# Performance work log

Measured on AMD Instinct MI355X. Metric: run time of the kernel, lower is better.

The kernel has to match this reference:

```python
import jax, jax.numpy as jnp
import numpy as np

D_IN = 256
DIMS = 256


def setup_inputs() -> dict:
    key = jax.random.key(0)
    k1, k2, k3, k4, k5 = jax.random.split(key, 5)
    B, Tq, Tk = 4, 512, 512
    query = jax.random.normal(k1, (B, Tq, D_IN), dtype=jnp.float32)
    value = jax.random.normal(k2, (B, Tk, D_IN), dtype=jnp.float32)
    # Dense(dims, use_bias=False) kernels (glorot-like scale) and AdditiveAttention scale vector
    Wq = jax.random.normal(k3, (D_IN, DIMS), dtype=jnp.float32) / np.sqrt(D_IN)
    Wv = jax.random.normal(k4, (D_IN, DIMS), dtype=jnp.float32) / np.sqrt(D_IN)
    scale = jax.random.normal(k5, (DIMS,), dtype=jnp.float32)
    return {"query": query, "value": value, "Wq": Wq, "Wv": Wv, "scale": scale}


def reference(query, value, Wq, Wv, scale):
    # q_proj: [B,Tq,d], k_proj: [B,Tk,d]; attention value = RAW value tensor (as in source)
    q = jnp.einsum("bqi,id->bqd", query, Wq)
    k = jnp.einsum("bki,id->bkd", value, Wv)
    # Additive (Bahdanau) scores: [B,Tq,Tk] via broadcast tanh then reduce with scale
    scores = jnp.einsum("bqkd,d->bqk", jnp.tanh(q[:, :, None, :] + k[:, None, :, :]), scale)
    attn = jax.nn.softmax(scores, axis=-1)  # masks are all-ones -> no-op
    out = jnp.einsum("bqk,bki->bqi", attn, value)
    return out, attn
```

## Files before the change

### kernel.cpp

```cpp
#include <hip/hip_runtime.h>

#define LOG2E 1.4426950408889634f
#define TWO_LOG2E 2.885390081777927f

__device__ __forceinline__ float fast_exp2(float x) { return __builtin_amdgcn_exp2f(x); }
__device__ __forceinline__ float fast_rcp(float x)  { return __builtin_amdgcn_rcpf(x); }

__global__ __launch_bounds__(256) void proj_kernel(
    const float* __restrict__ query, const float* __restrict__ value,
    const float* __restrict__ Wq, const float* __restrict__ Wv,
    float* __restrict__ eq, float* __restrict__ ek)
{
    __shared__ float in_lds[8 * 256];
    const int t = threadIdx.x;
    const int row0 = blockIdx.x * 8;
    const float* src; const float* W; float* dst;
    if (row0 < 2048) { src = query + (size_t)row0 * 256; W = Wq; dst = eq + (size_t)row0 * 256; }
    else { const int r = row0 - 2048; src = value + (size_t)r * 256; W = Wv; dst = ek + (size_t)r * 256; }

    const float4* s4 = (const float4*)src;
    float4* l4 = (float4*)in_lds;
    l4[t] = s4[t];
    l4[t + 256] = s4[t + 256];
    __syncthreads();

    float acc[8];
#pragma unroll
    for (int r = 0; r < 8; ++r) acc[r] = 0.f;

    for (int d = 0; d < 256; d += 4) {
        const float w0 = W[(d + 0) * 256 + t];
        const float w1 = W[(d + 1) * 256 + t];
        const float w2 = W[(d + 2) * 256 + t];
        const float w3 = W[(d + 3) * 256 + t];
#pragma unroll
        for (int r = 0; r < 8; ++r) {
            const float4 v = *(const float4*)&in_lds[r * 256 + d];
            acc[r] = fmaf(v.x, w0, acc[r]);
            acc[r] = fmaf(v.y, w1, acc[r]);
            acc[r] = fmaf(v.z, w2, acc[r]);
            acc[r] = fmaf(v.w, w3, acc[r]);
        }
    }
#pragma unroll
    for (int r = 0; r < 8; ++r) dst[r * 256 + t] = fast_exp2(acc[r] * TWO_LOG2E);
}

#define SQ_ST 130
__global__ __launch_bounds__(256) void scores_kernel(
    const float* __restrict__ eq, const float* __restrict__ ek,
    const float* __restrict__ scale,
    float* __restrict__ part0, float* __restrict__ part1)
{
    __shared__ float q_lds[32 * SQ_ST];
    __shared__ float k_lds[32 * SQ_ST];
    __shared__ float sc_lds[128];

    const int t = threadIdx.x;
    const int tx = t & 15, ty = t >> 4;
    const int kt = blockIdx.x, qt = blockIdx.y;
    const int b = blockIdx.z >> 1, dh = blockIdx.z & 1;
    const int d0 = dh * 128;
    const float* qbase = eq + (size_t)(b * 512 + qt * 32) * 256 + d0;
    const float* kbase = ek + (size_t)(b * 512 + kt * 32) * 256 + d0;

    if (t < 128) sc_lds[t] = -2.f * scale[d0 + t];

#pragma unroll
    for (int l = 0; l < 4; ++l) {
        const int idx = t + 256 * l;
        const int row = idx >> 5, c4 = (idx & 31) * 4;
        const float4 qv = *(const float4*)&qbase[row * 256 + c4];
        const float4 kv = *(const float4*)&kbase[row * 256 + c4];
        *(float2*)&q_lds[row * SQ_ST + c4]     = make_float2(qv.x, qv.y);
        *(float2*)&q_lds[row * SQ_ST + c4 + 2] = make_float2(qv.z, qv.w);
        *(float2*)&k_lds[row * SQ_ST + c4]     = make_float2(kv.x, kv.y);
        *(float2*)&k_lds[row * SQ_ST + c4 + 2] = make_float2(kv.z, kv.w);
    }
    __syncthreads();

    float a00 = 0.f, a01 = 0.f, a10 = 0.f, a11 = 0.f;

#pragma unroll 4
    for (int d = 0; d < 128; d += 2) {
        const float2 s2 = *(const float2*)&sc_lds[d];
        const float2 qa = *(const float2*)&q_lds[(ty * 2 + 0) * SQ_ST + d];
        const float2 qb = *(const float2*)&q_lds[(ty * 2 + 1) * SQ_ST + d];
        const float2 ka = *(const float2*)&k_lds[(tx * 2 + 0) * SQ_ST + d];
        const float2 kb = *(const float2*)&k_lds[(tx * 2 + 1) * SQ_ST + d];

        {
            const float A = fmaf(qa.x, ka.x, 1.f), B = fmaf(qa.y, ka.y, 1.f);
            a00 = fmaf(fmaf(s2.y, A, s2.x * B), fast_rcp(A * B), a00);
        }
        {
            const float A = fmaf(qa.x, kb.x, 1.f), B = fmaf(qa.y, kb.y, 1.f);
            a01 = fmaf(fmaf(s2.y, A, s2.x * B), fast_rcp(A * B), a01);
        }
        {
            const float A = fmaf(qb.x, ka.x, 1.f), B = fmaf(qb.y, ka.y, 1.f);
            a10 = fmaf(fmaf(s2.y, A, s2.x * B), fast_rcp(A * B), a10);
        }
        {
            const float A = fmaf(qb.x, kb.x, 1.f), B = fmaf(qb.y, kb.y, 1.f);
            a11 = fmaf(fmaf(s2.y, A, s2.x * B), fast_rcp(A * B), a11);
        }
    }

    float* part = dh ? part1 : part0;
    const int qrow = qt * 32 + ty * 2;
    const int kcol = kt * 32 + tx * 2;
    *(float2*)&part[(size_t)(b * 512 + qrow + 0) * 512 + kcol] = make_float2(a00, a01);
    *(float2*)&part[(size_t)(b * 512 + qrow + 1) * 512 + kcol] = make_float2(a10, a11);
}

__global__ __launch_bounds__(64) void softmax_kernel(
    const float* __restrict__ part0, const float* __restrict__ part1,
    float* __restrict__ attn)
{
    const int row = blockIdx.x;
    const float4* p0 = (const float4*)(part0 + (size_t)row * 512);
    const float4* p1 = (const float4*)(part1 + (size_t)row * 512);
    float4* po = (float4*)(attn + (size_t)row * 512);
    const int t = threadIdx.x;

    float4 a = p0[t], a2 = p1[t];
    a.x += a2.x; a.y += a2.y; a.z += a2.z; a.w += a2.w;
    float4 b = p0[t + 64], b2 = p1[t + 64];
    b.x += b2.x; b.y += b2.y; b.z += b2.z; b.w += b2.w;

    float m = fmaxf(fmaxf(fmaxf(a.x, a.y), fmaxf(a.z, a.w)),
                    fmaxf(fmaxf(b.x, b.y), fmaxf(b.z, b.w)));
#pragma unroll
    for (int off = 32; off; off >>= 1) m = fmaxf(m, __shfl_xor(m, off));

    a.x = fast_exp2((a.x - m) * LOG2E); a.y = fast_exp2((a.y - m) * LOG2E);
    a.z = fast_exp2((a.z - m) * LOG2E); a.w = fast_exp2((a.w - m) * LOG2E);
    b.x = fast_exp2((b.x - m) * LOG2E); b.y = fast_exp2((b.y - m) * LOG2E);
    b.z = fast_exp2((b.z - m) * LOG2E); b.w = fast_exp2((b.w - m) * LOG2E);

    float sum = ((a.x + a.y) + (a.z + a.w)) + ((b.x + b.y) + (b.z + b.w));
#pragma unroll
    for (int off = 32; off; off >>= 1) sum += __shfl_xor(sum, off);

    const float inv = fast_rcp(sum);
    a.x *= inv; a.y *= inv; a.z *= inv; a.w *= inv;
    b.x *= inv; b.y *= inv; b.z *= inv; b.w *= inv;
    po[t] = a; po[t + 64] = b;
}

#define AT_ST 68
#define VT_ST 68
__global__ __launch_bounds__(256) void pv_kernel(
    const float* __restrict__ attn, const float* __restrict__ value,
    float* __restrict__ out)
{
    __shared__ float a_lds[32 * AT_ST];
    __shared__ float v_lds[64 * VT_ST];

    const int t = threadIdx.x;
    const int tx = t & 15, ty = t >> 4;
    const int b = blockIdx.z, qt = blockIdx.y, it = blockIdx.x;
    const int q0 = qt * 32, i0 = it * 64;
    const float* abase = attn + (size_t)(b * 512 + q0) * 512;
    const float* vbase = value + (size_t)(b * 512) * 256 + i0;

    float4 acc0 = {0, 0, 0, 0}, acc1 = {0, 0, 0, 0};

    for (int kc = 0; kc < 512; kc += 64) {
        __syncthreads();
#pragma unroll
        for (int l = 0; l < 2; ++l) {
            const int f = t + 256 * l;
            const int row = f >> 4, c4 = (f & 15) * 4;
            *(float4*)&a_lds[row * AT_ST + c4] = *(const float4*)&abase[row * 512 + kc + c4];
        }
#pragma unroll
        for (int l = 0; l < 4; ++l) {
            const int f = t + 256 * l;
            const int row = f >> 4, c4 = (f & 15) * 4;
            *(float4*)&v_lds[row * VT_ST + c4] = *(const float4*)&vbase[(size_t)(kc + row) * 256 + c4];
        }
        __syncthreads();

        for (int k = 0; k < 64; ++k) {
            const float a0 = a_lds[(ty * 2 + 0) * AT_ST + k];
            const float a1 = a_lds[(ty * 2 + 1) * AT_ST + k];
            const float4 v = *(const float4*)&v_lds[k * VT_ST + tx * 4];
            acc0.x = fmaf(a0, v.x, acc0.x); acc0.y = fmaf(a0, v.y, acc0.y);
            acc0.z = fmaf(a0, v.z, acc0.z); acc0.w = fmaf(a0, v.w, acc0.w);
            acc1.x = fmaf(a1, v.x, acc1.x); acc1.y = fmaf(a1, v.y, acc1.y);
            acc1.z = fmaf(a1, v.z, acc1.z); acc1.w = fmaf(a1, v.w, acc1.w);
        }
    }

    float* obase = out + (size_t)(b * 512 + q0) * 256 + i0;
    *(float4*)&obase[(ty * 2 + 0) * 256 + tx * 4] = acc0;
    *(float4*)&obase[(ty * 2 + 1) * 256 + tx * 4] = acc1;
}

extern "C" void kernel_launch(void* const* d_in, const int* in_sizes, int n_in,
                              void* d_out, int out_size, void* d_ws, size_t ws_size,
                              hipStream_t stream) {
    const float* query = (const float*)d_in[0];
    const float* value = (const float*)d_in[1];
    const float* Wq    = (const float*)d_in[2];
    const float* Wv    = (const float*)d_in[3];
    const float* scale = (const float*)d_in[4];

    float* out0 = (float*)d_out;
    float* attn = out0 + 4 * 512 * 256;

    float* eq    = (float*)d_ws;
    float* ek    = eq + 2048 * 256;
    float* part0 = ek + 2048 * 256;
    float* part1 = part0 + 4 * 512 * 512;

    proj_kernel<<<512, 256, 0, stream>>>(query, value, Wq, Wv, eq, ek);
    scores_kernel<<<dim3(16, 16, 8), 256, 0, stream>>>(eq, ek, scale, part0, part1);
    softmax_kernel<<<2048, 64, 0, stream>>>(part0, part1, attn);
    pv_kernel<<<dim3(4, 16, 4), 256, 0, stream>>>(attn, value, out0);
}
```

Measured before the change: 73.11 us.

## Fuse softmax and attention-value product into one kernel

Merges the softmax and PV kernels so each block normalizes 8 query rows in LDS and immediately multiplies the unnormalized exponentials by value, applying 1/sum at the end. This removes a kernel launch and the global reread of the attention matrix. In exchange every block stages the full value tile for its batch in a large LDS buffer, limiting occupancy and increasing L2 traffic, with less register reuse per thread.

```diff
diff --git a/kernel.cpp b/kernel.cpp
--- a/kernel.cpp
+++ b/kernel.cpp
@@ -114,89 +114,95 @@
     *(float2*)&part[(size_t)(b * 512 + qrow + 1) * 512 + kcol] = make_float2(a10, a11);
 }
 
-__global__ __launch_bounds__(64) void softmax_kernel(
+#define ST_ROW 516
+__global__ __launch_bounds__(512) void softpv_kernel(
     const float* __restrict__ part0, const float* __restrict__ part1,
-    float* __restrict__ attn)
+    const float* __restrict__ value,
+    float* __restrict__ attn, float* __restrict__ out)
 {
-    const int row = blockIdx.x;
-    const float4* p0 = (const float4*)(part0 + (size_t)row * 512);
-    const float4* p1 = (const float4*)(part1 + (size_t)row * 512);
-    float4* po = (float4*)(attn + (size_t)row * 512);
+    __shared__ float s_tile[8 * ST_ROW];
+    __shared__ float v_lds[64 * 256];
+    __shared__ float inv_lds[8];
+
     const int t = threadIdx.x;
-
-    float4 a = p0[t], a2 = p1[t];
-    a.x += a2.x; a.y += a2.y; a.z += a2.z; a.w += a2.w;
-    float4 b = p0[t + 64], b2 = p1[t + 64];
-    b.x += b2.x; b.y += b2.y; b.z += b2.z; b.w += b2.w;
-
-    float m = fmaxf(fmaxf(fmaxf(a.x, a.y), fmaxf(a.z, a.w)),
-                    fmaxf(fmaxf(b.x, b.y), fmaxf(b.z, b.w)));
-#pragma unroll
-    for (int off = 32; off; off >>= 1) m = fmaxf(m, __shfl_xor(m, off));
-
-    a.x = fast_exp2((a.x - m) * LOG2E); a.y = fast_exp2((a.y - m) * LOG2E);
-    a.z = fast_exp2((a.z - m) * LOG2E); a.w = fast_exp2((a.w - m) * LOG2E);
-    b.x = fast_exp2((b.x - m) * LOG2E); b.y = fast_exp2((b.y - m) * LOG2E);
-    b.z = fast_exp2((b.z - m) * LOG2E); b.w = fast_exp2((b.w - m) * LOG2E);
-
-    float sum = ((a.x + a.y) + (a.z + a.w)) + ((b.x + b.y) + (b.z + b.w));
-#pragma unroll
-    for (int off = 32; off; off >>= 1) sum += __shfl_xor(sum, off);
-
-    const float inv = fast_rcp(sum);
-    a.x *= inv; a.y *= inv; a.z *= inv; a.w *= inv;
-    b.x *= inv; b.y *= inv; b.z *= inv; b.w *= inv;
-    po[t] = a; po[t + 64] = b;
-}
-
-#define AT_ST 68
-#define VT_ST 68
-__global__ __launch_bounds__(256) void pv_kernel(
-    const float* __restrict__ attn, const float* __restrict__ value,
-    float* __restrict__ out)
-{
-    __shared__ float a_lds[32 * AT_ST];
-    __shared__ float v_lds[64 * VT_ST];
-
-    const int t = threadIdx.x;
-    const int tx = t & 15, ty = t >> 4;
-    const int b = blockIdx.z, qt = blockIdx.y, it = blockIdx.x;
-    const int q0 = qt * 32, i0 = it * 64;
-    const float* abase = attn + (size_t)(b * 512 + q0) * 512;
-    const float* vbase = value + (size_t)(b * 512) * 256 + i0;
-
-    float4 acc0 = {0, 0, 0, 0}, acc1 = {0, 0, 0, 0};
+    const int qt = blockIdx.x, b = blockIdx.y;
+    const int q0 = qt * 8;
+    const size_t rowbase = (size_t)(b * 512 + q0) * 512;
+
+    {
+        const float4* p0 = (const float4*)(part0 + rowbase);
+        const float4* p1 = (const float4*)(part1 + rowbase);
+#pragma unroll
+        for (int l = 0; l < 2; ++l) {
+            const int idx = t + 512 * l;
+            const int row = idx >> 7, c4 = idx & 127;
+            float4 a = p0[idx];
+            const float4 c = p1[idx];
+            a.x += c.x; a.y += c.y; a.z += c.z; a.w += c.w;
+            *(float4*)&s_tile[row * ST_ROW + c4 * 4] = a;
+        }
+    }
+    __syncthreads();
+
+    const int w = t >> 6, lane = t & 63;
+    {
+        float e[8];
+        float m = -1e30f;
+#pragma unroll
+        for (int j = 0; j < 8; ++j) {
+            e[j] = s_tile[w * ST_ROW + lane + 64 * j];
+            m = fmaxf(m, e[j]);
+        }
+#pragma unroll
+        for (int off = 32; off; off >>= 1) m = fmaxf(m, __shfl_xor(m, off));
+
+        float sum = 0.f;
+#pragma unroll
+        for (int j = 0; j < 8; ++j) {
+            e[j] = fast_exp2((e[j] - m) * LOG2E);
+            sum += e[j];
+        }
+#pragma unroll
+        for (int off = 32; off; off >>= 1) sum += __shfl_xor(sum, off);
+
+        const float inv = fast_rcp(sum);
+        float* arow = attn + rowbase + (size_t)w * 512;
+#pragma unroll
+        for (int j = 0; j < 8; ++j) {
+            s_tile[w * ST_ROW + lane + 64 * j] = e[j];
+            arow[lane + 64 * j] = e[j] * inv;
+        }
+        if (lane == 0) inv_lds[w] = inv;
+    }
+
+    const int r = lane >> 3;
+    const int c = 32 * w + (lane & 7) * 4;
+    float4 acc = {0.f, 0.f, 0.f, 0.f};
 
     for (int kc = 0; kc < 512; kc += 64) {
         __syncthreads();
-#pragma unroll
-        for (int l = 0; l < 2; ++l) {
-            const int f = t + 256 * l;
-            const int row = f >> 4, c4 = (f & 15) * 4;
-            *(float4*)&a_lds[row * AT_ST + c4] = *(const float4*)&abase[row * 512 + kc + c4];
-        }
-#pragma unroll
-        for (int l = 0; l < 4; ++l) {
-            const int f = t + 256 * l;
-            const int row = f >> 4, c4 = (f & 15) * 4;
-            *(float4*)&v_lds[row * VT_ST + c4] = *(const float4*)&vbase[(size_t)(kc + row) * 256 + c4];
+        const float4* vsrc = (const float4*)(value + (size_t)(b * 512 + kc) * 256);
+#pragma unroll
+        for (int l = 0; l < 8; ++l) {
+            const int idx = t + 512 * l;
+            *(float4*)&v_lds[idx * 4] = vsrc[idx];
         }
         __syncthreads();
 
+#pragma unroll 4
         for (int k = 0; k < 64; ++k) {
-            const float a0 = a_lds[(ty * 2 + 0) * AT_ST + k];
-            const float a1 = a_lds[(ty * 2 + 1) * AT_ST + k];
-            const float4 v = *(const float4*)&v_lds[k * VT_ST + tx * 4];
-            acc0.x = fmaf(a0, v.x, acc0.x); acc0.y = fmaf(a0, v.y, acc0.y);
-            acc0.z = fmaf(a0, v.z, acc0.z); acc0.w = fmaf(a0, v.w, acc0.w);
-            acc1.x = fmaf(a1, v.x, acc1.x); acc1.y = fmaf(a1, v.y, acc1.y);
-            acc1.z = fmaf(a1, v.z, acc1.z); acc1.w = fmaf(a1, v.w, acc1.w);
-        }
-    }
-
-    float* obase = out + (size_t)(b * 512 + q0) * 256 + i0;
-    *(float4*)&obase[(ty * 2 + 0) * 256 + tx * 4] = acc0;
-    *(float4*)&obase[(ty * 2 + 1) * 256 + tx * 4] = acc1;
+            const float s = s_tile[r * ST_ROW + kc + k];
+            const float4 v = *(const float4*)&v_lds[k * 256 + c];
+            acc.x = fmaf(s, v.x, acc.x);
+            acc.y = fmaf(s, v.y, acc.y);
+            acc.z = fmaf(s, v.z, acc.z);
+            acc.w = fmaf(s, v.w, acc.w);
+        }
+    }
+
+    const float inv = inv_lds[r];
+    acc.x *= inv; acc.y *= inv; acc.z *= inv; acc.w *= inv;
+    *(float4*)&out[(size_t)(b * 512 + q0 + r) * 256 + c] = acc;
 }
 
 extern "C" void kernel_launch(void* const* d_in, const int* in_sizes, int n_in,
@@ -218,6 +224,5 @@
 
     proj_kernel<<<512, 256, 0, stream>>>(query, value, Wq, Wv, eq, ek);
     scores_kernel<<<dim3(16, 16, 8), 256, 0, stream>>>(eq, ek, scale, part0, part1);
-    softmax_kernel<<<2048, 64, 0, stream>>>(part0, part1, attn);
-    pv_kernel<<<dim3(4, 16, 4), 256, 0, stream>>>(attn, value, out0);
-}
+    softpv_kernel<<<dim3(64, 4), 512, 0, stream>>>(part0, part1, value, attn, out0);
+}
```

Result: slower. 75.56 us (+3.4%).
